# Optimization experiments

Hardware: AMD Instinct MI355X
Metric: run time of the kernel (lower is better)

## Reference

```python
import jax, jax.numpy as jnp
import numpy as np

B, S, D = 8, 2048, 512


def setup_inputs() -> dict:
    key = jax.random.key(0)
    ks = jax.random.split(key, 8)
    x = jax.random.normal(ks[0], (B, S, D), dtype=jnp.float32)
    mask = jax.random.randint(ks[1], (B, S, 1), 0, 2, dtype=jnp.int32)
    Wq = jax.random.normal(ks[2], (D, D), dtype=jnp.float32) / np.sqrt(D)
    bq = jax.random.normal(ks[3], (D,), dtype=jnp.float32) * 0.01
    Wk = jax.random.normal(ks[4], (D, D), dtype=jnp.float32) / np.sqrt(D)
    bk = jax.random.normal(ks[5], (D,), dtype=jnp.float32) * 0.01
    Wv = jax.random.normal(ks[6], (D, D), dtype=jnp.float32) / np.sqrt(D)
    bv = jax.random.normal(ks[7], (D,), dtype=jnp.float32) * 0.01
    return {"x": x, "mask": mask, "Wq": Wq, "bq": bq, "Wk": Wk, "bk": bk, "Wv": Wv, "bv": bv}


def reference(x, mask, Wq, bq, Wk, bk, Wv, bv):
    # torch Linear: y = x @ W^T + b
    Q = jnp.einsum('bsd,ed->bse', x, Wq) + bq
    K = jnp.einsum('bsd,ed->bse', x, Wk) + bk
    V = jnp.einsum('bsd,ed->bse', x, Wv) + bv
    scale = 1.0 / jnp.sqrt(jnp.asarray(x.shape[-1], dtype=x.dtype))
    scores = jnp.einsum('bqd,bkd->bqk', Q, K) * scale  # [B, S, S]
    attn_mask = jnp.transpose(mask, (0, 2, 1))  # [B, 1, S], broadcasts over queries
    scores = jnp.where(attn_mask == 0, jnp.asarray(-10000.0, dtype=scores.dtype), scores)
    attn = jax.nn.softmax(scores, axis=-1)
    return jnp.einsum('bqk,bkd->bqd', attn, V)
```

## Files before the change

kernel.cpp:

```cpp
#include <hip/hip_runtime.h>
#include <cstddef>

#define BB 8
#define SS 2048
#define DD 512
#define MM (BB * SS)

typedef __attribute__((ext_vector_type(8))) short bf16x8;
typedef __attribute__((ext_vector_type(4))) float f32x4;
typedef __attribute__((ext_vector_type(4))) unsigned short u16x4;

__device__ __forceinline__ f32x4 mfma16(bf16x8 a, bf16x8 b, f32x4 c) {
  return __builtin_amdgcn_mfma_f32_16x16x32_bf16(a, b, c, 0, 0, 0);
}
__device__ __forceinline__ unsigned short f2bf(float f) {
  unsigned int u = __float_as_uint(f);
  u += 0x7fffu + ((u >> 16) & 1u);
  return (unsigned short)(u >> 16);
}
__device__ __forceinline__ void gld16(const void* g, void* l) {
  __builtin_amdgcn_global_load_lds((const __attribute__((address_space(1))) void*)g,
                                   (__attribute__((address_space(3))) void*)l, 16, 0, 0);
}

__global__ void cvt_bf16_kernel(const float* __restrict__ in,
                                unsigned short* __restrict__ out, int n4) {
  int i = blockIdx.x * blockDim.x + threadIdx.x;
  if (i >= n4) return;
  f32x4 v = reinterpret_cast<const f32x4*>(in)[i];
  u16x4 o;
  o[0] = f2bf(v[0]);
  o[1] = f2bf(v[1]);
  o[2] = f2bf(v[2]);
  o[3] = f2bf(v[3]);
  reinterpret_cast<u16x4*>(out)[i] = o;
}
__global__ void cvt_w3_kernel(const float* __restrict__ s0, const float* __restrict__ s1,
                              const float* __restrict__ s2, unsigned short* __restrict__ d0,
                              unsigned short* __restrict__ d1, unsigned short* __restrict__ d2) {
  const float* s = blockIdx.y == 0 ? s0 : (blockIdx.y == 1 ? s1 : s2);
  unsigned short* d = blockIdx.y == 0 ? d0 : (blockIdx.y == 1 ? d1 : d2);
  int i = blockIdx.x * blockDim.x + threadIdx.x;
  f32x4 v = reinterpret_cast<const f32x4*>(s)[i];
  u16x4 o;
  o[0] = f2bf(v[0]);
  o[1] = f2bf(v[1]);
  o[2] = f2bf(v[2]);
  o[3] = f2bf(v[3]);
  reinterpret_cast<u16x4*>(d)[i] = o;
}

__global__ void mask_scan_kernel(const int* __restrict__ mask, int* __restrict__ idx,
                                 int* __restrict__ nbArr) {
  __shared__ int part[256];
  const int b = blockIdx.x;
  const int t = threadIdx.x;
  int m[8], c = 0;
#pragma unroll
  for (int e = 0; e < 8; ++e) {
    m[e] = mask[b * SS + t * 8 + e];
    c += (m[e] != 0);
  }
  int v = c;
  part[t] = v;
  __syncthreads();
  for (int off = 1; off < 256; off <<= 1) {
    int u = (t >= off) ? part[t - off] : 0;
    __syncthreads();
    v += u;
    part[t] = v;
    __syncthreads();
  }
  int base = v - c;
#pragma unroll
  for (int e = 0; e < 8; ++e)
    if (m[e]) idx[b * SS + base++] = t * 8 + e;
  const int nb = part[255];
  if (t == 255) nbArr[b] = nb;
  for (int j = nb + t; j < SS; j += 256) idx[b * SS + j] = 0;
}

__global__ __launch_bounds__(256, 2) void qkv_gemm_kernel(
    const unsigned short* __restrict__ X, const unsigned short* __restrict__ W0,
    const unsigned short* __restrict__ W1, const unsigned short* __restrict__ W2,
    const float* __restrict__ b0, const float* __restrict__ b1,
    const float* __restrict__ b2, unsigned short* __restrict__ O0,
    unsigned short* __restrict__ O1, unsigned short* __restrict__ O2) {
  __shared__ unsigned char a_lds[2][128 * 128];
  __shared__ unsigned char b_lds[2][128 * 128];
  const int tid = threadIdx.x;
  const int w = tid >> 6, l = tid & 63, lr = l & 15, hi = l >> 4;
  const int which = blockIdx.y >> 2;
  const unsigned short* W = which == 0 ? W0 : (which == 1 ? W1 : W2);
  const float* bias = which == 0 ? b0 : (which == 1 ? b1 : b2);
  unsigned short* out = which == 0 ? O0 : (which == 1 ? O1 : O2);
  const float oscale = which == 0 ? 0.044194173824159216f : 1.0f;
  const int m0 = blockIdx.x * 128;
  const int n0 = (blockIdx.y & 3) * 128;
  const int wm = (w >> 1) * 64, wn = (w & 1) * 64;
  const int srow = l >> 3, gchunk = (l & 7) ^ (srow & 7);

  f32x4 acc[4][4];
#pragma unroll
  for (int mt = 0; mt < 4; ++mt)
#pragma unroll
    for (int nt = 0; nt < 4; ++nt) acc[mt][nt] = (f32x4){0.f, 0.f, 0.f, 0.f};

  const unsigned short* ga = X + (size_t)(m0 + w * 32 + srow) * DD + gchunk * 8;
  const unsigned short* gb = W + (size_t)(n0 + w * 32 + srow) * DD + gchunk * 8;

  for (int k0 = 0; k0 < DD; k0 += 128) {
#pragma unroll
    for (int ii = 0; ii < 4; ++ii) {
      gld16(ga + (size_t)ii * 8 * DD + k0, &a_lds[0][(w * 4 + ii) * 1024]);
      gld16(gb + (size_t)ii * 8 * DD + k0, &b_lds[0][(w * 4 + ii) * 1024]);
      gld16(ga + (size_t)ii * 8 * DD + k0 + 64, &a_lds[1][(w * 4 + ii) * 1024]);
      gld16(gb + (size_t)ii * 8 * DD + k0 + 64, &b_lds[1][(w * 4 + ii) * 1024]);
    }
    __syncthreads();
#pragma unroll
    for (int hf = 0; hf < 2; ++hf) {
#pragma unroll
      for (int dkl = 0; dkl < 2; ++dkl) {
        const int gc = dkl * 4 + hi;
        bf16x8 af[4], bfr[4];
#pragma unroll
        for (int mt = 0; mt < 4; ++mt) {
          const int row = wm + mt * 16 + lr;
          af[mt] = *reinterpret_cast<const bf16x8*>(
              &a_lds[hf][row * 128 + ((gc ^ (row & 7)) * 16)]);
        }
#pragma unroll
        for (int nt = 0; nt < 4; ++nt) {
          const int row = wn + nt * 16 + lr;
          bfr[nt] = *reinterpret_cast<const bf16x8*>(
              &b_lds[hf][row * 128 + ((gc ^ (row & 7)) * 16)]);
        }
#pragma unroll
        for (int mt = 0; mt < 4; ++mt)
#pragma unroll
          for (int nt = 0; nt < 4; ++nt)
            acc[mt][nt] = mfma16(af[mt], bfr[nt], acc[mt][nt]);
      }
    }
    __syncthreads();
  }

#pragma unroll
  for (int nt = 0; nt < 4; ++nt) {
    const int col = n0 + wn + nt * 16 + lr;
    const float bv = bias[col];
#pragma unroll
    for (int mt = 0; mt < 4; ++mt)
#pragma unroll
      for (int r = 0; r < 4; ++r) {
        const int row = m0 + wm + mt * 16 + hi * 4 + r;
        out[(size_t)row * DD + col] = f2bf((acc[mt][nt][r] + bv) * oscale);
      }
  }
}

__global__ void vtrans_kernel(const unsigned short* __restrict__ V,
                              const int* __restrict__ idx, const int* __restrict__ nbArr,
                              unsigned short* __restrict__ VT2) {
  __shared__ unsigned short t[64][72];
  const int b = blockIdx.z;
  const int kt = blockIdx.x;
  const int d0 = blockIdx.y * 64;
  const int tid = threadIdx.x;
  const int c = tid & 63, rg = tid >> 6;
  const int nb = nbArr[b];
#pragma unroll
  for (int i = 0; i < 16; ++i) {
    const int row = rg * 16 + i;
    const int s = kt * 64 + row;
    const int src = s < nb ? idx[b * SS + s] : 0;
    t[row][c] = V[((size_t)b * SS + src) * DD + d0 + c];
  }
  __syncthreads();
#pragma unroll
  for (int i = 0; i < 16; ++i) {
    const int ix = i * 256 + tid;
    const int jj = ix & 7;
    const int dl = (ix >> 3) & 63;
    const int cc = ix >> 9;
    VT2[(((size_t)(b * 32 + kt) * 8 + cc) * 512 + d0 + dl) * 8 + jj] =
        t[cc * 8 + jj][dl];
  }
}

__global__ __launch_bounds__(256, 2) void attn_kernel(
    const unsigned short* __restrict__ Q, const unsigned short* __restrict__ K,
    const unsigned short* __restrict__ VT2, const int* __restrict__ idx,
    const int* __restrict__ nbArr, float* __restrict__ Out,
    float* __restrict__ Apart, float* __restrict__ mlpart) {
  __shared__ unsigned char k_lds[32 * 1024];
  __shared__ unsigned char vt_lds[4 * 512 * 16];
  __shared__ unsigned short pbuf[4][16][32];
  __shared__ int ids[1024];
  const int tid = threadIdx.x;
  const int w = tid >> 6, l = tid & 63, lr = l & 15, hi = l >> 4;
  const int bid = blockIdx.x;
  const int b = bid & 7;
  const int qt = (bid >> 3) >> 1;
  const int sp = (bid >> 3) & 1;
  const int q0 = qt * 64 + w * 16;

  const int nb = nbArr[b];
  const int ntile = (nb + 31) >> 5;
  const int half = (ntile + 1) >> 1;
  const int lo = sp == 0 ? 0 : half;
  const int hi_t = sp == 0 ? half : ntile;
  const int ntl = hi_t - lo;

  const unsigned short* __restrict__ Qb = Q + (size_t)b * SS * DD;
  const unsigned short* __restrict__ Kb = K + (size_t)b * SS * DD;
  const unsigned short* __restrict__ Vb = VT2 + (size_t)b * SS * DD;
  const int* __restrict__ idxb = idx + b * SS;

  for (int j = tid; j < ntl * 32; j += 256) ids[j] = idxb[lo * 32 + j];

  bf16x8 qf[16];
#pragma unroll
  for (int dk = 0; dk < 16; ++dk)
    qf[dk] = *reinterpret_cast<const bf16x8*>(
        &Qb[(size_t)(q0 + lr) * DD + dk * 32 + hi * 8]);

  f32x4 oacc[32];
#pragma unroll
  for (int i = 0; i < 32; ++i) oacc[i] = (f32x4){0.f, 0.f, 0.f, 0.f};
  float mrow[4], lrow[4];
#pragma unroll
  for (int r = 0; r < 4; ++r) {
    mrow[r] = -10000.0f;
    lrow[r] = 0.0f;
  }

  __syncthreads();

  for (int t = lo; t < hi_t; ++t) {
    const int tr = t - lo;
#pragma unroll
    for (int r = 0; r < 8; ++r) {
      const int row = w * 8 + r;
      const int src = ids[tr * 32 + row];
      const int ch = (l & 56) | ((l ^ row) & 7);
      gld16(Kb + (size_t)src * DD + ch * 8, &k_lds[row * 1024]);
    }
    const size_t vbase = ((size_t)((t >> 1) * 8 + (t & 1) * 4 + w) * 512);
#pragma unroll
    for (int g = 0; g < 8; ++g)
      gld16(Vb + (vbase + g * 64 + l) * 8, &vt_lds[(w * 512 + g * 64) * 16]);
    __syncthreads();

    f32x4 sacc[2];
#pragma unroll
    for (int nt = 0; nt < 2; ++nt) sacc[nt] = (f32x4){0.f, 0.f, 0.f, 0.f};
#pragma unroll
    for (int dk = 0; dk < 16; ++dk) {
#pragma unroll
      for (int nt = 0; nt < 2; ++nt) {
        const int row = nt * 16 + lr;
        const int c = dk * 4 + hi;
        bf16x8 bk = *reinterpret_cast<const bf16x8*>(
            &k_lds[row * 1024 + ((c & ~7) | ((c ^ row) & 7)) * 16]);
        sacc[nt] = mfma16(qf[dk], bk, sacc[nt]);
      }
    }

    float s[2][4];
#pragma unroll
    for (int nt = 0; nt < 2; ++nt) {
      const int j = t * 32 + nt * 16 + lr;
      const bool ok = j < nb;
#pragma unroll
      for (int r = 0; r < 4; ++r)
        s[nt][r] = ok ? sacc[nt][r] : -10000.0f;
    }

    float mx[4];
    float need = -1e30f;
#pragma unroll
    for (int r = 0; r < 4; ++r) {
      float m2 = fmaxf(s[0][r], s[1][r]);
#pragma unroll
      for (int off = 1; off < 16; off <<= 1) m2 = fmaxf(m2, __shfl_xor(m2, off));
      mx[r] = m2;
      need = fmaxf(need, m2 - mrow[r]);
    }
    if (__any(need > 8.0f)) {
#pragma unroll
      for (int r = 0; r < 4; ++r) {
        const float mnew = fmaxf(mrow[r], mx[r]);
        const float alpha = __expf(mrow[r] - mnew);
        mrow[r] = mnew;
        lrow[r] *= alpha;
#pragma unroll
        for (int nt2 = 0; nt2 < 32; ++nt2) oacc[nt2][r] *= alpha;
      }
    }
    float rs[4] = {0.f, 0.f, 0.f, 0.f};
#pragma unroll
    for (int nt = 0; nt < 2; ++nt)
#pragma unroll
      for (int r = 0; r < 4; ++r) {
        float p = __expf(s[nt][r] - mrow[r]);
        s[nt][r] = p;
        rs[r] += p;
      }
#pragma unroll
    for (int r = 0; r < 4; ++r) {
      float tt = rs[r];
#pragma unroll
      for (int off = 1; off < 16; off <<= 1) tt += __shfl_xor(tt, off);
      lrow[r] += tt;
    }

#pragma unroll
    for (int nt = 0; nt < 2; ++nt)
#pragma unroll
      for (int r = 0; r < 4; ++r)
        pbuf[w][hi * 4 + r][nt * 16 + lr] = f2bf(s[nt][r]);
    bf16x8 pf = *reinterpret_cast<const bf16x8*>(&pbuf[w][lr][hi * 8]);

#pragma unroll
    for (int nt2 = 0; nt2 < 32; ++nt2) {
      bf16x8 v0 = *reinterpret_cast<const bf16x8*>(
          &vt_lds[(hi * 512 + nt2 * 16 + lr) * 16]);
      oacc[nt2] = mfma16(pf, v0, oacc[nt2]);
    }
    __syncthreads();
  }

  float* Ap = sp == 0 ? Out : Apart;
#pragma unroll
  for (int nt2 = 0; nt2 < 32; ++nt2)
#pragma unroll
    for (int r = 0; r < 4; ++r)
      Ap[((size_t)b * SS + q0 + hi * 4 + r) * DD + nt2 * 16 + lr] = oacc[nt2][r];
  if (lr == 0) {
#pragma unroll
    for (int r = 0; r < 4; ++r) {
      const size_t row = (size_t)sp * MM + b * SS + q0 + hi * 4 + r;
      mlpart[row * 2 + 0] = mrow[r];
      mlpart[row * 2 + 1] = lrow[r];
    }
  }
}

__global__ void combine_kernel(float* __restrict__ Out, const float* __restrict__ Apart,
                               const float* __restrict__ mlpart) {
  const int gid = blockIdx.x * 256 + threadIdx.x;
  const int row = gid >> 7;
  const float m1 = mlpart[(size_t)row * 2 + 0];
  const float l1 = mlpart[(size_t)row * 2 + 1];
  const float m2 = mlpart[((size_t)MM + row) * 2 + 0];
  const float l2 = mlpart[((size_t)MM + row) * 2 + 1];
  const float m = fmaxf(m1, m2);
  const float w1 = __expf(m1 - m), w2 = __expf(m2 - m);
  const float inv = 1.0f / (w1 * l1 + w2 * l2);
  f32x4 a1 = reinterpret_cast<f32x4*>(Out)[gid];
  f32x4 a2 = reinterpret_cast<const f32x4*>(Apart)[gid];
  f32x4 o;
#pragma unroll
  for (int e = 0; e < 4; ++e) o[e] = (w1 * a1[e] + w2 * a2[e]) * inv;
  reinterpret_cast<f32x4*>(Out)[gid] = o;
}

extern "C" void kernel_launch(void* const* d_in, const int* in_sizes, int n_in,
                              void* d_out, int out_size, void* d_ws, size_t ws_size,
                              hipStream_t stream) {
  const float* x = (const float*)d_in[0];
  const int* mask = (const int*)d_in[1];
  const float* Wq = (const float*)d_in[2];
  const float* bq = (const float*)d_in[3];
  const float* Wk = (const float*)d_in[4];
  const float* bk = (const float*)d_in[5];
  const float* Wv = (const float*)d_in[6];
  const float* bv = (const float*)d_in[7];
  float* out = (float*)d_out;

  char* ws = (char*)d_ws;
  const size_t MB = 1024 * 1024;
  unsigned short* Qb = (unsigned short*)(ws);
  unsigned short* Kb = (unsigned short*)(ws + 16 * MB);
  unsigned short* VT2b = (unsigned short*)(ws + 32 * MB);
  unsigned short* Xb = (unsigned short*)(ws + 48 * MB);
  unsigned short* Vb = (unsigned short*)(ws + 64 * MB);
  float* Apart = (float*)(ws + 48 * MB);
  unsigned short* Wqb = (unsigned short*)(ws + 80 * MB);
  unsigned short* Wkb = Wqb + 512 * 512;
  unsigned short* Wvb = Wkb + 512 * 512;
  int* idx = (int*)(ws + 82 * MB);
  int* nbArr = (int*)(ws + 82 * MB + 65536);
  float* mlpart = (float*)(ws + 82 * MB + 128 * 1024);

  cvt_bf16_kernel<<<8192, 256, 0, stream>>>(x, Xb, (MM * DD) / 4);
  cvt_w3_kernel<<<dim3(256, 3), 256, 0, stream>>>(Wq, Wk, Wv, Wqb, Wkb, Wvb);
  mask_scan_kernel<<<BB, 256, 0, stream>>>(mask, idx, nbArr);

  qkv_gemm_kernel<<<dim3(MM / 128, 12), 256, 0, stream>>>(
      Xb, Wqb, Wkb, Wvb, bq, bk, bv, Qb, Kb, Vb);

  vtrans_kernel<<<dim3(SS / 64, DD / 64, BB), 256, 0, stream>>>(Vb, idx, nbArr, VT2b);

  attn_kernel<<<512, 256, 0, stream>>>(Qb, Kb, VT2b, idx, nbArr, out, Apart, mlpart);

  combine_kernel<<<(MM * DD / 4) / 256, 256, 0, stream>>>(out, Apart, mlpart);
}
```

Before: 244.5 us.

## Add 8-wave attention kernel with four-way key split and four-part combine

Adds an attention kernel with 512-thread blocks (8 waves of 16 query rows each, 128 queries per block) that splits the unmasked key range four ways instead of two. Partial outputs go to three extra workspace buffers and are merged by a new four-way combine kernel. It also skips the online-softmax rescale unless the row max grows by more than 8. The new path runs only when the workspace is at least 150 MB and falls back to the old kernels otherwise. In exchange it adds more partial-output traffic and a heavier combine pass.

```diff
diff --git a/kernel.cpp b/kernel.cpp
--- a/kernel.cpp
+++ b/kernel.cpp
@@ -348,6 +348,168 @@
   }
 }
 
+__global__ __launch_bounds__(512, 4) void attn8_kernel(
+    const unsigned short* __restrict__ Q, const unsigned short* __restrict__ K,
+    const unsigned short* __restrict__ VT2, const int* __restrict__ idx,
+    const int* __restrict__ nbArr, float* __restrict__ Out,
+    float* __restrict__ A1, float* __restrict__ A2, float* __restrict__ A3,
+    float* __restrict__ mlpart) {
+  __shared__ unsigned char k_lds[32 * 1024];
+  __shared__ unsigned char vt_lds[4 * 512 * 16];
+  __shared__ unsigned short pbuf[8][16][32];
+  __shared__ int ids[1024];
+  const int tid = threadIdx.x;
+  const int w = tid >> 6, l = tid & 63, lr = l & 15, hi = l >> 4;
+  const int bid = blockIdx.x;
+  const int b = bid & 7;
+  const int sp = (bid >> 3) & 3;
+  const int qt = bid >> 5;
+  const int q0 = qt * 128 + w * 16;
+
+  const int nb = nbArr[b];
+  const int ntile = (nb + 31) >> 5;
+  const int lo = (ntile * sp) >> 2;
+  const int hi_t = (ntile * (sp + 1)) >> 2;
+  const int ntl = hi_t - lo;
+
+  const unsigned short* __restrict__ Qb = Q + (size_t)b * SS * DD;
+  const unsigned short* __restrict__ Kb = K + (size_t)b * SS * DD;
+  const unsigned short* __restrict__ Vb = VT2 + (size_t)b * SS * DD;
+  const int* __restrict__ idxb = idx + b * SS;
+
+  for (int j = tid; j < ntl * 32; j += 512) ids[j] = idxb[lo * 32 + j];
+
+  bf16x8 qf[16];
+#pragma unroll
+  for (int dk = 0; dk < 16; ++dk)
+    qf[dk] = *reinterpret_cast<const bf16x8*>(
+        &Qb[(size_t)(q0 + lr) * DD + dk * 32 + hi * 8]);
+
+  f32x4 oacc[32];
+#pragma unroll
+  for (int i = 0; i < 32; ++i) oacc[i] = (f32x4){0.f, 0.f, 0.f, 0.f};
+  float mrow[4], lrow[4];
+#pragma unroll
+  for (int r = 0; r < 4; ++r) {
+    mrow[r] = -10000.0f;
+    lrow[r] = 0.0f;
+  }
+
+  __syncthreads();
+
+  for (int t = lo; t < hi_t; ++t) {
+    const int tr = t - lo;
+#pragma unroll
+    for (int r = 0; r < 4; ++r) {
+      const int row = w * 4 + r;
+      const int src = ids[tr * 32 + row];
+      const int ch = (l & 56) | ((l ^ row) & 7);
+      gld16(Kb + (size_t)src * DD + ch * 8, &k_lds[row * 1024]);
+    }
+    const int c2 = w >> 1;
+    const size_t vbase = ((size_t)((t >> 1) * 8 + (t & 1) * 4 + c2) * 512);
+#pragma unroll
+    for (int gg = 0; gg < 4; ++gg) {
+      const int g = (w & 1) * 4 + gg;
+      gld16(Vb + (vbase + (size_t)g * 64 + l) * 8, &vt_lds[(c2 * 512 + g * 64) * 16]);
+    }
+    __syncthreads();
+
+    f32x4 sacc[2];
+#pragma unroll
+    for (int nt = 0; nt < 2; ++nt) sacc[nt] = (f32x4){0.f, 0.f, 0.f, 0.f};
+#pragma unroll
+    for (int dk = 0; dk < 16; ++dk) {
+#pragma unroll
+      for (int nt = 0; nt < 2; ++nt) {
+        const int row = nt * 16 + lr;
+        const int c = dk * 4 + hi;
+        bf16x8 bk = *reinterpret_cast<const bf16x8*>(
+            &k_lds[row * 1024 + ((c & ~7) | ((c ^ row) & 7)) * 16]);
+        sacc[nt] = mfma16(qf[dk], bk, sacc[nt]);
+      }
+    }
+
+    float s[2][4];
+#pragma unroll
+    for (int nt = 0; nt < 2; ++nt) {
+      const int j = t * 32 + nt * 16 + lr;
+      const bool ok = j < nb;
+#pragma unroll
+      for (int r = 0; r < 4; ++r)
+        s[nt][r] = ok ? sacc[nt][r] : -10000.0f;
+    }
+
+    float mx[4];
+    float need = -1e30f;
+#pragma unroll
+    for (int r = 0; r < 4; ++r) {
+      float m2 = fmaxf(s[0][r], s[1][r]);
+#pragma unroll
+      for (int off = 1; off < 16; off <<= 1) m2 = fmaxf(m2, __shfl_xor(m2, off));
+      mx[r] = m2;
+      need = fmaxf(need, m2 - mrow[r]);
+    }
+    if (__any(need > 8.0f)) {
+#pragma unroll
+      for (int r = 0; r < 4; ++r) {
+        const float mnew = fmaxf(mrow[r], mx[r]);
+        const float alpha = __expf(mrow[r] - mnew);
+        mrow[r] = mnew;
+        lrow[r] *= alpha;
+#pragma unroll
+        for (int nt2 = 0; nt2 < 32; ++nt2) oacc[nt2][r] *= alpha;
+      }
+    }
+    float rs[4] = {0.f, 0.f, 0.f, 0.f};
+#pragma unroll
+    for (int nt = 0; nt < 2; ++nt)
+#pragma unroll
+      for (int r = 0; r < 4; ++r) {
+        float p = __expf(s[nt][r] - mrow[r]);
+        s[nt][r] = p;
+        rs[r] += p;
+      }
+#pragma unroll
+    for (int r = 0; r < 4; ++r) {
+      float tt = rs[r];
+#pragma unroll
+      for (int off = 1; off < 16; off <<= 1) tt += __shfl_xor(tt, off);
+      lrow[r] += tt;
+    }
+
+#pragma unroll
+    for (int nt = 0; nt < 2; ++nt)
+#pragma unroll
+      for (int r = 0; r < 4; ++r)
+        pbuf[w][hi * 4 + r][nt * 16 + lr] = f2bf(s[nt][r]);
+    bf16x8 pf = *reinterpret_cast<const bf16x8*>(&pbuf[w][lr][hi * 8]);
+
+#pragma unroll
+    for (int nt2 = 0; nt2 < 32; ++nt2) {
+      bf16x8 v0 = *reinterpret_cast<const bf16x8*>(
+          &vt_lds[(hi * 512 + nt2 * 16 + lr) * 16]);
+      oacc[nt2] = mfma16(pf, v0, oacc[nt2]);
+    }
+    __syncthreads();
+  }
+
+  float* Ap = sp == 0 ? Out : (sp == 1 ? A1 : (sp == 2 ? A2 : A3));
+#pragma unroll
+  for (int nt2 = 0; nt2 < 32; ++nt2)
+#pragma unroll
+    for (int r = 0; r < 4; ++r)
+      Ap[((size_t)b * SS + q0 + hi * 4 + r) * DD + nt2 * 16 + lr] = oacc[nt2][r];
+  if (lr == 0) {
+#pragma unroll
+    for (int r = 0; r < 4; ++r) {
+      const size_t row = (size_t)sp * MM + b * SS + q0 + hi * 4 + r;
+      mlpart[row * 2 + 0] = mrow[r];
+      mlpart[row * 2 + 1] = lrow[r];
+    }
+  }
+}
+
 __global__ void combine_kernel(float* __restrict__ Out, const float* __restrict__ Apart,
                                const float* __restrict__ mlpart) {
   const int gid = blockIdx.x * 256 + threadIdx.x;
@@ -367,6 +529,37 @@
   reinterpret_cast<f32x4*>(Out)[gid] = o;
 }
 
+__global__ void combine4_kernel(float* __restrict__ Out, const float* __restrict__ A1,
+                                const float* __restrict__ A2, const float* __restrict__ A3,
+                                const float* __restrict__ mlpart) {
+  const int gid = blockIdx.x * 256 + threadIdx.x;
+  const int row = gid >> 7;
+  float mm[4], ll[4];
+  float m = -1e30f;
+#pragma unroll
+  for (int sp = 0; sp < 4; ++sp) {
+    mm[sp] = mlpart[((size_t)sp * MM + row) * 2 + 0];
+    ll[sp] = mlpart[((size_t)sp * MM + row) * 2 + 1];
+    m = fmaxf(m, mm[sp]);
+  }
+  float wgt[4], wsum = 0.f;
+#pragma unroll
+  for (int sp = 0; sp < 4; ++sp) {
+    wgt[sp] = __expf(mm[sp] - m);
+    wsum += wgt[sp] * ll[sp];
+  }
+  const float inv = 1.0f / wsum;
+  f32x4 a0 = reinterpret_cast<f32x4*>(Out)[gid];
+  f32x4 a1 = reinterpret_cast<const f32x4*>(A1)[gid];
+  f32x4 a2 = reinterpret_cast<const f32x4*>(A2)[gid];
+  f32x4 a3 = reinterpret_cast<const f32x4*>(A3)[gid];
+  f32x4 o;
+#pragma unroll
+  for (int e = 0; e < 4; ++e)
+    o[e] = (wgt[0] * a0[e] + wgt[1] * a1[e] + wgt[2] * a2[e] + wgt[3] * a3[e]) * inv;
+  reinterpret_cast<f32x4*>(Out)[gid] = o;
+}
+
 extern "C" void kernel_launch(void* const* d_in, const int* in_sizes, int n_in,
                               void* d_out, int out_size, void* d_ws, size_t ws_size,
                               hipStream_t stream) {
@@ -387,13 +580,17 @@
   unsigned short* VT2b = (unsigned short*)(ws + 32 * MB);
   unsigned short* Xb = (unsigned short*)(ws + 48 * MB);
   unsigned short* Vb = (unsigned short*)(ws + 64 * MB);
-  float* Apart = (float*)(ws + 48 * MB);
+  float* A1 = (float*)(ws + 48 * MB);
   unsigned short* Wqb = (unsigned short*)(ws + 80 * MB);
   unsigned short* Wkb = Wqb + 512 * 512;
   unsigned short* Wvb = Wkb + 512 * 512;
   int* idx = (int*)(ws + 82 * MB);
   int* nbArr = (int*)(ws + 82 * MB + 65536);
   float* mlpart = (float*)(ws + 82 * MB + 128 * 1024);
+  float* A2 = (float*)(ws + 84 * MB);
+  float* A3 = (float*)(ws + 116 * MB);
+
+  const bool big = ws_size >= (size_t)150 * MB;
 
   cvt_bf16_kernel<<<8192, 256, 0, stream>>>(x, Xb, (MM * DD) / 4);
   cvt_w3_kernel<<<dim3(256, 3), 256, 0, stream>>>(Wq, Wk, Wv, Wqb, Wkb, Wvb);
@@ -404,7 +601,12 @@
 
   vtrans_kernel<<<dim3(SS / 64, DD / 64, BB), 256, 0, stream>>>(Vb, idx, nbArr, VT2b);
 
-  attn_kernel<<<512, 256, 0, stream>>>(Qb, Kb, VT2b, idx, nbArr, out, Apart, mlpart);
-
-  combine_kernel<<<(MM * DD / 4) / 256, 256, 0, stream>>>(out, Apart, mlpart);
-}
+  if (big) {
+    attn8_kernel<<<512, 512, 0, stream>>>(Qb, Kb, VT2b, idx, nbArr, out, A1, A2, A3,
+                                          mlpart);
+    combine4_kernel<<<(MM * DD / 4) / 256, 256, 0, stream>>>(out, A1, A2, A3, mlpart);
+  } else {
+    attn_kernel<<<512, 256, 0, stream>>>(Qb, Kb, VT2b, idx, nbArr, out, A1, mlpart);
+    combine_kernel<<<(MM * DD / 4) / 256, 256, 0, stream>>>(out, A1, mlpart);
+  }
+}
```

After: 852.2 us. +248.6%, slower.

## Fuse prep kernels into one launch and overlap V loads with QK compute

Applied to the files above, without the earlier changes.

Merges the x conversion, weight conversion and mask scan into a single prep kernel, dispatched by block index, to cut launch overhead. In the attention loop, the single barrier after issuing the K and V loads becomes a partial wait on K only (vmcnt(8)). A second wait for V is placed just before the PV MFMAs. This lets the V tile transfer overlap the QK score and softmax computation, but it relies on correct vmcnt accounting of the load order.

```diff
diff --git a/kernel.cpp b/kernel.cpp
--- a/kernel.cpp
+++ b/kernel.cpp
@@ -23,38 +23,42 @@
                                    (__attribute__((address_space(3))) void*)l, 16, 0, 0);
 }
 
-__global__ void cvt_bf16_kernel(const float* __restrict__ in,
-                                unsigned short* __restrict__ out, int n4) {
-  int i = blockIdx.x * blockDim.x + threadIdx.x;
-  if (i >= n4) return;
-  f32x4 v = reinterpret_cast<const f32x4*>(in)[i];
-  u16x4 o;
-  o[0] = f2bf(v[0]);
-  o[1] = f2bf(v[1]);
-  o[2] = f2bf(v[2]);
-  o[3] = f2bf(v[3]);
-  reinterpret_cast<u16x4*>(out)[i] = o;
-}
-__global__ void cvt_w3_kernel(const float* __restrict__ s0, const float* __restrict__ s1,
-                              const float* __restrict__ s2, unsigned short* __restrict__ d0,
-                              unsigned short* __restrict__ d1, unsigned short* __restrict__ d2) {
-  const float* s = blockIdx.y == 0 ? s0 : (blockIdx.y == 1 ? s1 : s2);
-  unsigned short* d = blockIdx.y == 0 ? d0 : (blockIdx.y == 1 ? d1 : d2);
-  int i = blockIdx.x * blockDim.x + threadIdx.x;
-  f32x4 v = reinterpret_cast<const f32x4*>(s)[i];
-  u16x4 o;
-  o[0] = f2bf(v[0]);
-  o[1] = f2bf(v[1]);
-  o[2] = f2bf(v[2]);
-  o[3] = f2bf(v[3]);
-  reinterpret_cast<u16x4*>(d)[i] = o;
-}
-
-__global__ void mask_scan_kernel(const int* __restrict__ mask, int* __restrict__ idx,
-                                 int* __restrict__ nbArr) {
+__global__ void prep_kernel(const float* __restrict__ x, unsigned short* __restrict__ Xb,
+                            const float* __restrict__ Wq, const float* __restrict__ Wk,
+                            const float* __restrict__ Wv, unsigned short* __restrict__ Wqb,
+                            unsigned short* __restrict__ Wkb, unsigned short* __restrict__ Wvb,
+                            const int* __restrict__ mask, int* __restrict__ idx,
+                            int* __restrict__ nbArr) {
   __shared__ int part[256];
-  const int b = blockIdx.x;
+  const int bx = blockIdx.x;
   const int t = threadIdx.x;
+  if (bx < 8192) {
+    const int i = bx * 256 + t;
+    f32x4 v = reinterpret_cast<const f32x4*>(x)[i];
+    u16x4 o;
+    o[0] = f2bf(v[0]);
+    o[1] = f2bf(v[1]);
+    o[2] = f2bf(v[2]);
+    o[3] = f2bf(v[3]);
+    reinterpret_cast<u16x4*>(Xb)[i] = o;
+    return;
+  }
+  if (bx < 8960) {
+    const int k = bx - 8192;
+    const int which = k >> 8;
+    const float* s = which == 0 ? Wq : (which == 1 ? Wk : Wv);
+    unsigned short* d = which == 0 ? Wqb : (which == 1 ? Wkb : Wvb);
+    const int i = (k & 255) * 256 + t;
+    f32x4 v = reinterpret_cast<const f32x4*>(s)[i];
+    u16x4 o;
+    o[0] = f2bf(v[0]);
+    o[1] = f2bf(v[1]);
+    o[2] = f2bf(v[2]);
+    o[3] = f2bf(v[3]);
+    reinterpret_cast<u16x4*>(d)[i] = o;
+    return;
+  }
+  const int b = bx - 8960;
   int m[8], c = 0;
 #pragma unroll
   for (int e = 0; e < 8; ++e) {
@@ -251,7 +255,9 @@
 #pragma unroll
     for (int g = 0; g < 8; ++g)
       gld16(Vb + (vbase + g * 64 + l) * 8, &vt_lds[(w * 512 + g * 64) * 16]);
-    __syncthreads();
+
+    asm volatile("s_waitcnt vmcnt(8)" ::: "memory");
+    __builtin_amdgcn_s_barrier();
 
     f32x4 sacc[2];
 #pragma unroll
@@ -322,6 +328,9 @@
       for (int r = 0; r < 4; ++r)
         pbuf[w][hi * 4 + r][nt * 16 + lr] = f2bf(s[nt][r]);
     bf16x8 pf = *reinterpret_cast<const bf16x8*>(&pbuf[w][lr][hi * 8]);
+
+    asm volatile("s_waitcnt vmcnt(0)" ::: "memory");
+    __builtin_amdgcn_s_barrier();
 
 #pragma unroll
     for (int nt2 = 0; nt2 < 32; ++nt2) {
@@ -395,9 +404,8 @@
   int* nbArr = (int*)(ws + 82 * MB + 65536);
   float* mlpart = (float*)(ws + 82 * MB + 128 * 1024);
 
-  cvt_bf16_kernel<<<8192, 256, 0, stream>>>(x, Xb, (MM * DD) / 4);
-  cvt_w3_kernel<<<dim3(256, 3), 256, 0, stream>>>(Wq, Wk, Wv, Wqb, Wkb, Wvb);
-  mask_scan_kernel<<<BB, 256, 0, stream>>>(mask, idx, nbArr);
+  prep_kernel<<<8968, 256, 0, stream>>>(x, Xb, Wq, Wk, Wv, Wqb, Wkb, Wvb, mask, idx,
+                                        nbArr);
 
   qkv_gemm_kernel<<<dim3(MM / 128, 12), 256, 0, stream>>>(
       Xb, Wqb, Wkb, Wvb, bq, bk, bv, Qb, Kb, Vb);
```

After: 242.8 us. About the same (-0.7%).
